# Kernel optimization log

Hardware: AMD Instinct MI355X
Metric: run time of the kernel (lower is better)

## Reference

```python
import jax, jax.numpy as jnp
import numpy as np

B, H, HKV, QLEN, KVLEN, D = 4, 32, 8, 16, 8192, 128


def setup_inputs() -> dict:
    key = jax.random.key(0)
    ks = jax.random.split(key, 7)
    query = jax.random.normal(ks[0], (B, H, QLEN, D), dtype=jnp.float32)
    # INT8 KV caches (stored as int8, dequantized in the hot path)
    key_cache = jax.random.randint(ks[1], (B, HKV, KVLEN, D), -127, 128).astype(jnp.int8)
    value_cache = jax.random.randint(ks[2], (B, HKV, KVLEN, D), -127, 128).astype(jnp.int8)
    # per-(batch, kv_head, token) quant params, broadcast over head_dim
    key_scale = jax.random.uniform(ks[3], (B, HKV, KVLEN), dtype=jnp.float32, minval=0.005, maxval=0.02)
    key_zero = jax.random.normal(ks[4], (B, HKV, KVLEN), dtype=jnp.float32)
    value_scale = jax.random.uniform(ks[5], (B, HKV, KVLEN), dtype=jnp.float32, minval=0.005, maxval=0.02)
    value_zero = jax.random.normal(ks[6], (B, HKV, KVLEN), dtype=jnp.float32)
    return {
        "query": query,
        "key_cache": key_cache,
        "value_cache": value_cache,
        "key_scale": key_scale,
        "key_zero": key_zero,
        "value_scale": value_scale,
        "value_zero": value_zero,
    }


def _dequant(x_q, scale, zero, dtype):
    # (x_q - zero) * scale, params broadcast over head_dim
    return ((x_q.astype(jnp.float32) - zero[..., None]) * scale[..., None]).astype(dtype)


def reference(query, key_cache, value_cache, key_scale, key_zero, value_scale, value_zero):
    b, h, qlen, d = query.shape
    hkv = key_cache.shape[1]
    n_rep = h // hkv  # GQA: each kv head serves n_rep query heads
    scale = jnp.asarray(d, query.dtype) ** -0.5

    k = _dequant(key_cache, key_scale, key_zero, query.dtype)   # [b, hkv, kv, d]
    v = _dequant(value_cache, value_scale, value_zero, query.dtype)

    # Grouped einsum == repeat_interleave of K/V along heads, without materializing copies
    qg = query.reshape(b, hkv, n_rep, qlen, d)
    scores = jnp.einsum('bgrqd,bgkd->bgrqk', qg, k) * scale      # [b, hkv, n_rep, q, kv]
    attn = jax.nn.softmax(scores, axis=-1)
    out = jnp.einsum('bgrqk,bgkd->bgrqd', attn, v)
    return out.reshape(b, h, qlen, d)
```

## Files before the change

kernel.cpp:

```cpp
#include <hip/hip_runtime.h>
#include <hip/hip_bf16.h>
#include <stdint.h>

#define Bc    4
#define Hc    32
#define HKVc  8
#define QLc   16
#define KVc   8192
#define Dc    128
#define NREPc 4
#define THR   8.0f

typedef _Float16 f16x8 __attribute__((ext_vector_type(8)));
typedef _Float16 f16x4 __attribute__((ext_vector_type(4)));
typedef float f32x4  __attribute__((ext_vector_type(4)));
typedef int   i32x4  __attribute__((ext_vector_type(4)));
typedef uint32_t u32x2 __attribute__((ext_vector_type(2)));

__device__ __forceinline__ uint32_t pk1152(int x0, int x1) {
  return (__builtin_amdgcn_perm((uint32_t)x1, (uint32_t)x0, 0x05040100u)
          & 0x00FF00FFu) ^ 0x64806480u;
}

#define BAR() do {                                            \
    asm volatile("s_waitcnt lgkmcnt(0)" ::: "memory");        \
    __builtin_amdgcn_sched_barrier(0);                        \
    __builtin_amdgcn_s_barrier();                             \
  } while (0)

__global__ __launch_bounds__(256) void attn_partial(
    const float* __restrict__ q, const int* __restrict__ kc,
    const int* __restrict__ vc,
    const float* __restrict__ ksc, const float* __restrict__ kzr,
    const float* __restrict__ vsc, const float* __restrict__ vzr,
    float* __restrict__ ws_acc, float* __restrict__ ws_m,
    float* __restrict__ ws_l, int nsplit)
{
  __shared__ __align__(16) unsigned short Klds[2][32][128];
  __shared__ __align__(16) unsigned short Vlds[2][128][36];
  __shared__ __align__(16) float          Sl[4][256];

  const int bid   = blockIdx.x;
  const int split = bid % nsplit;
  const int bg    = bid / nsplit;
  const int chunk = KVc / nsplit;
  const int t_begin = split * chunk;
  const int nt    = chunk >> 5;

  const int tid  = threadIdx.x;
  const int wave = tid >> 6;
  const int lane = tid & 63;
  const int l15  = lane & 15;
  const int lg   = lane >> 4;

  const int b = bg >> 3, g = bg & 7;
  const int h = (g << 2) + wave;

  f16x8 qa[4];
  float qsum = 0.f;
  const float* qrow = q + ((size_t)((b * Hc + h) * QLc + l15)) * Dc;
#pragma unroll
  for (int ks = 0; ks < 4; ++ks) {
    const f32x4* qv = (const f32x4*)(qrow + ks * 32 + (lg << 3));
    f32x4 qlo = qv[0], qhi = qv[1];
    f16x8 f;
#pragma unroll
    for (int j = 0; j < 4; ++j) {
      f[j]     = (_Float16)qlo[j];
      f[4 + j] = (_Float16)qhi[j];
      qsum += (float)f[j] + (float)f[4 + j];
    }
    qa[ks] = f;
  }
  qsum += __shfl_xor(qsum, 16);
  qsum += __shfl_xor(qsum, 32);

  const float QK_SCALE = 0.088388347648f * 1.44269504089f;

  float m = -1e30f, ell = 0.f, corr = 0.f;
  f32x4 acc[8];
#pragma unroll
  for (int dt = 0; dt < 8; ++dt) acc[dt] = (f32x4){0.f, 0.f, 0.f, 0.f};

  const int*   kb   = kc  + (size_t)bg * KVc * Dc;
  const int*   vb   = vc  + (size_t)bg * KVc * Dc;
  const float* kscb = ksc + (size_t)bg * KVc;
  const float* kzrb = kzr + (size_t)bg * KVc;
  const float* vscb = vsc + (size_t)bg * KVc;
  const float* vzrb = vzr + (size_t)bg * KVc;

  const int kt  = tid >> 3;
  const int kd  = (tid & 7) << 4;
  const int ksw = (kt & 7) << 3;
  const int tq  = tid >> 5;
  const int dq  = (tid & 31) << 2;
  const int tb  = (tq << 2) ^ ((((dq >> 4) & 3)) << 3);

  i32x4 kpA[4], vpA[4], kpB[4], vpB[4];

#define ISSUE(KP, VP, TILE) do {                                             \
    const int _t0 = t_begin + ((TILE) << 5);                                 \
    const int* _ks = kb + (size_t)(_t0 + kt) * Dc + kd;                      \
    KP[0] = ((const i32x4*)_ks)[0]; KP[1] = ((const i32x4*)_ks)[1];          \
    KP[2] = ((const i32x4*)_ks)[2]; KP[3] = ((const i32x4*)_ks)[3];          \
    VP[0] = *(const i32x4*)(vb + (size_t)(_t0 + (tq << 2) + 0) * Dc + dq);   \
    VP[1] = *(const i32x4*)(vb + (size_t)(_t0 + (tq << 2) + 1) * Dc + dq);   \
    VP[2] = *(const i32x4*)(vb + (size_t)(_t0 + (tq << 2) + 2) * Dc + dq);   \
    VP[3] = *(const i32x4*)(vb + (size_t)(_t0 + (tq << 2) + 3) * Dc + dq);   \
  } while (0)

#define WRITE(KP, VP, BUF) do {                                              \
    i32x4 _kA, _kB;                                                          \
    _kA[0]=(int)pk1152(KP[0][0],KP[0][1]); _kA[1]=(int)pk1152(KP[0][2],KP[0][3]); \
    _kA[2]=(int)pk1152(KP[1][0],KP[1][1]); _kA[3]=(int)pk1152(KP[1][2],KP[1][3]); \
    _kB[0]=(int)pk1152(KP[2][0],KP[2][1]); _kB[1]=(int)pk1152(KP[2][2],KP[2][3]); \
    _kB[2]=(int)pk1152(KP[3][0],KP[3][1]); _kB[3]=(int)pk1152(KP[3][2],KP[3][3]); \
    *(i32x4*)&Klds[BUF][kt][kd ^ ksw]       = _kA;                           \
    *(i32x4*)&Klds[BUF][kt][(kd + 8) ^ ksw] = _kB;                           \
    _Pragma("unroll")                                                        \
    for (int _j = 0; _j < 4; ++_j) {                                         \
      u32x2 _pk;                                                             \
      _pk[0] = pk1152(VP[0][_j], VP[1][_j]);                                 \
      _pk[1] = pk1152(VP[2][_j], VP[3][_j]);                                 \
      *(u32x2*)&Vlds[BUF][dq + _j][tb] = _pk;                                \
    }                                                                        \
  } while (0)

#define RESTAGE(WBASE) do {                                                  \
    const int _arr = tid >> 6;                                               \
    const int _sl  = (tid & 63) << 2;                                        \
    int _toff = _sl;                                                         \
    if (_toff > chunk - 4) _toff = chunk - 4;                                \
    const float* _sp = (_arr == 0) ? kscb : (_arr == 1) ? kzrb               \
                     : (_arr == 2) ? vscb : vzrb;                            \
    f32x4 _sv = *(const f32x4*)(_sp + (WBASE) + _toff);                      \
    if (_arr == 0) { _sv[0]*=QK_SCALE; _sv[1]*=QK_SCALE;                     \
                     _sv[2]*=QK_SCALE; _sv[3]*=QK_SCALE; }                   \
    else if (_arr == 2) { _sv[0]*=1024.f; _sv[1]*=1024.f;                    \
                          _sv[2]*=1024.f; _sv[3]*=1024.f; }                  \
    else { _sv[0]+=1152.f; _sv[1]+=1152.f; _sv[2]+=1152.f; _sv[3]+=1152.f; } \
    *(f32x4*)&Sl[_arr][_sl] = _sv;                                           \
  } while (0)

  ISSUE(kpA, vpA, 0);
  RESTAGE(t_begin);
  WRITE(kpA, vpA, 0);
  if (nt > 1) ISSUE(kpA, vpA, 1);
  if (nt > 2) ISSUE(kpB, vpB, 2);
  BAR();

  for (int it = 0; it < nt; ++it) {
    const int cur = it & 1;

    if (it && !(it & 7)) {
      RESTAGE(t_begin + ((it >> 3) << 8));
      BAR();
    }

    if (it + 1 < nt) {
      if ((it + 1) & 1) {
        WRITE(kpA, vpA, cur ^ 1);
        if (it + 3 < nt) ISSUE(kpA, vpA, it + 3);
      } else {
        WRITE(kpB, vpB, cur ^ 1);
        if (it + 3 < nt) ISSUE(kpB, vpB, it + 3);
      }
    }

    const int tw = (it & 7) << 5;
    const f32x4 ksc0 = *(const f32x4*)&Sl[0][tw + (lg << 2)];
    const f32x4 ksc1 = *(const f32x4*)&Sl[0][tw + 16 + (lg << 2)];
    const f32x4 kzr0 = *(const f32x4*)&Sl[1][tw + (lg << 2)];
    const f32x4 kzr1 = *(const f32x4*)&Sl[1][tw + 16 + (lg << 2)];
    const f32x4 vsc0 = *(const f32x4*)&Sl[2][tw + (lg << 2)];
    const f32x4 vsc1 = *(const f32x4*)&Sl[2][tw + 16 + (lg << 2)];
    const f32x4 vzr0 = *(const f32x4*)&Sl[3][tw + (lg << 2)];
    const f32x4 vzr1 = *(const f32x4*)&Sl[3][tw + 16 + (lg << 2)];

    f32x4 sA0 = (f32x4){0.f,0.f,0.f,0.f}, sA1 = (f32x4){0.f,0.f,0.f,0.f};
    f32x4 sB0 = (f32x4){0.f,0.f,0.f,0.f}, sB1 = (f32x4){0.f,0.f,0.f,0.f};
    __builtin_amdgcn_s_setprio(1);
#pragma unroll
    for (int ks = 0; ks < 2; ++ks) {
      f16x8 kfA = *(const f16x8*)
          &Klds[cur][l15][(ks * 32 + (lg << 3)) ^ ((l15 & 7) << 3)];
      sA0 = __builtin_amdgcn_mfma_f32_16x16x32_f16(kfA, qa[ks], sA0, 0, 0, 0);
      f16x8 kfB = *(const f16x8*)
          &Klds[cur][16 + l15][(ks * 32 + (lg << 3)) ^ ((l15 & 7) << 3)];
      sB0 = __builtin_amdgcn_mfma_f32_16x16x32_f16(kfB, qa[ks], sB0, 0, 0, 0);
    }
#pragma unroll
    for (int ks = 2; ks < 4; ++ks) {
      f16x8 kfA = *(const f16x8*)
          &Klds[cur][l15][(ks * 32 + (lg << 3)) ^ ((l15 & 7) << 3)];
      sA1 = __builtin_amdgcn_mfma_f32_16x16x32_f16(kfA, qa[ks], sA1, 0, 0, 0);
      f16x8 kfB = *(const f16x8*)
          &Klds[cur][16 + l15][(ks * 32 + (lg << 3)) ^ ((l15 & 7) << 3)];
      sB1 = __builtin_amdgcn_mfma_f32_16x16x32_f16(kfB, qa[ks], sB1, 0, 0, 0);
    }
    __builtin_amdgcn_s_setprio(0);
    const f32x4 scA = sA0 + sA1;
    const f32x4 scB = sB0 + sB1;

    float s0[4], s1[4];
#pragma unroll
    for (int j = 0; j < 4; ++j) {
      s0[j] = ksc0[j] * (scA[j] - kzr0[j] * qsum);
      s1[j] = ksc1[j] * (scB[j] - kzr1[j] * qsum);
    }

    float tm = fmaxf(fmaxf(fmaxf(s0[0], s0[1]), fmaxf(s0[2], s0[3])),
                     fmaxf(fmaxf(s1[0], s1[1]), fmaxf(s1[2], s1[3])));
    tm = fmaxf(tm, __shfl_xor(tm, 16));
    tm = fmaxf(tm, __shfl_xor(tm, 32));
    if (__any(tm > m + THR)) {
      float nm = fmaxf(m, tm);
      float cf = exp2f(m - nm);
      m = nm;
      ell *= cf; corr *= cf;
      float cfq[4];
#pragma unroll
      for (int j = 0; j < 4; ++j) cfq[j] = __shfl(cf, (lg << 2) + j);
#pragma unroll
      for (int dt = 0; dt < 8; ++dt)
#pragma unroll
        for (int j = 0; j < 4; ++j) acc[dt][j] *= cfq[j];
    }

    f16x8 pp;
#pragma unroll
    for (int j = 0; j < 4; ++j) {
      float pA = exp2f(s0[j] - m);
      float pB = exp2f(s1[j] - m);
      ell += pA + pB;
      _Float16 ca = (_Float16)(pA * vsc0[j]);
      _Float16 cb = (_Float16)(pB * vsc1[j]);
      corr += (float)ca * vzr0[j] + (float)cb * vzr1[j];
      pp[j]     = ca;
      pp[4 + j] = cb;
    }

    __builtin_amdgcn_s_setprio(1);
#pragma unroll
    for (int dt = 0; dt < 8; ++dt) {
      const int swz = (dt & 3) << 3;
      f16x4 vA = *(const f16x4*)&Vlds[cur][(dt << 4) + l15][(lg << 2) ^ swz];
      f16x4 vB = *(const f16x4*)&Vlds[cur][(dt << 4) + l15][(16 + (lg << 2)) ^ swz];
      f16x8 vf = __builtin_shufflevector(vA, vB, 0, 1, 2, 3, 4, 5, 6, 7);
      acc[dt] = __builtin_amdgcn_mfma_f32_16x16x32_f16(pp, vf, acc[dt], 0, 0, 0);
    }
    __builtin_amdgcn_s_setprio(0);

    if (it + 1 < nt) BAR();
  }

  ell += __shfl_xor(ell, 16);  ell += __shfl_xor(ell, 32);
  corr += __shfl_xor(corr, 16); corr += __shfl_xor(corr, 32);
  float corrq[4];
#pragma unroll
  for (int j = 0; j < 4; ++j) corrq[j] = __shfl(corr, (lg << 2) + j);

  const size_t pbase = ((size_t)bg * nsplit + split) * 64;
  const float inv1k = 0.0009765625f;
#pragma unroll
  for (int dt = 0; dt < 8; ++dt)
#pragma unroll
    for (int j = 0; j < 4; ++j) {
      int row = (wave << 4) + (lg << 2) + j;
      int d   = (dt << 4) + l15;
      ws_acc[(pbase + row) * Dc + d] = (acc[dt][j] - corrq[j]) * inv1k;
    }
  if (lg == 0) {
    ws_m[pbase + (wave << 4) + l15] = m;
    ws_l[pbase + (wave << 4) + l15] = ell;
  }
#undef ISSUE
#undef WRITE
#undef RESTAGE
}

__global__ __launch_bounds__(128) void attn_combine(
    const float* __restrict__ ws_acc, const float* __restrict__ ws_m,
    const float* __restrict__ ws_l, float* __restrict__ out, int nsplit)
{
  const int r   = blockIdx.x;
  const int bg  = r >> 6;
  const int row = r & 63;
  const int d   = threadIdx.x;

  float M = -1e30f;
#pragma unroll 4
  for (int i = 0; i < nsplit; ++i)
    M = fmaxf(M, ws_m[((size_t)bg * nsplit + i) * 64 + row]);
  float L = 0.f, o = 0.f;
#pragma unroll 4
  for (int i = 0; i < nsplit; ++i) {
    size_t pb = ((size_t)bg * nsplit + i) * 64 + row;
    float w = exp2f(ws_m[pb] - M);
    L += ws_l[pb] * w;
    o += ws_acc[pb * Dc + d] * w;
  }
  const int b = bg >> 3, g = bg & 7;
  const int rep = row >> 4, qq = row & 15;
  out[(((size_t)(b * Hc + g * NREPc + rep)) * QLc + qq) * Dc + d] = o / L;
}

extern "C" void kernel_launch(void* const* d_in, const int* in_sizes, int n_in,
                              void* d_out, int out_size, void* d_ws,
                              size_t ws_size, hipStream_t stream) {
  const float* q   = (const float*)d_in[0];
  const int*   kc  = (const int*)d_in[1];
  const int*   vc  = (const int*)d_in[2];
  const float* ksc = (const float*)d_in[3];
  const float* kzr = (const float*)d_in[4];
  const float* vsc = (const float*)d_in[5];
  const float* vzr = (const float*)d_in[6];
  float* out = (float*)d_out;

  int nsplit = 32;
  while (nsplit > 1) {
    size_t need = (size_t)32 * nsplit * 64 * (Dc + 2) * sizeof(float);
    if (need <= ws_size) break;
    nsplit >>= 1;
  }
  float* ws_acc = (float*)d_ws;
  float* ws_m   = ws_acc + (size_t)32 * nsplit * 64 * Dc;
  float* ws_l   = ws_m   + (size_t)32 * nsplit * 64;

  attn_partial<<<dim3(32 * nsplit), dim3(256), 0, stream>>>(
      q, kc, vc, ksc, kzr, vsc, vzr, ws_acc, ws_m, ws_l, nsplit);
  attn_combine<<<dim3(32 * 64), dim3(128), 0, stream>>>(
      ws_acc, ws_m, ws_l, out, nsplit);
}
```

Before: 80.88 us.

## Process 64 KV tokens per iteration using both LDS buffers as one tile

```diff
diff --git a/kernel.cpp b/kernel.cpp
--- a/kernel.cpp
+++ b/kernel.cpp
@@ -45,7 +45,7 @@
   const int bg    = bid / nsplit;
   const int chunk = KVc / nsplit;
   const int t_begin = split * chunk;
-  const int nt    = chunk >> 5;
+  const int nt2   = chunk >> 6;
 
   const int tid  = threadIdx.x;
   const int wave = tid >> 6;
@@ -143,74 +143,59 @@
   } while (0)
 
   ISSUE(kpA, vpA, 0);
+  ISSUE(kpB, vpB, 1);
   RESTAGE(t_begin);
   WRITE(kpA, vpA, 0);
-  if (nt > 1) ISSUE(kpA, vpA, 1);
-  if (nt > 2) ISSUE(kpB, vpB, 2);
+  WRITE(kpB, vpB, 1);
+  if (nt2 > 1) { ISSUE(kpA, vpA, 2); ISSUE(kpB, vpB, 3); }
   BAR();
 
-  for (int it = 0; it < nt; ++it) {
-    const int cur = it & 1;
-
-    if (it && !(it & 7)) {
-      RESTAGE(t_begin + ((it >> 3) << 8));
+  for (int st = 0; st < nt2; ++st) {
+    if (st && !(st & 3)) {
+      RESTAGE(t_begin + ((st >> 2) << 8));
       BAR();
     }
 
-    if (it + 1 < nt) {
-      if ((it + 1) & 1) {
-        WRITE(kpA, vpA, cur ^ 1);
-        if (it + 3 < nt) ISSUE(kpA, vpA, it + 3);
-      } else {
-        WRITE(kpB, vpB, cur ^ 1);
-        if (it + 3 < nt) ISSUE(kpB, vpB, it + 3);
-      }
-    }
-
-    const int tw = (it & 7) << 5;
+    const int tw = (st & 3) << 6;
     const f32x4 ksc0 = *(const f32x4*)&Sl[0][tw + (lg << 2)];
     const f32x4 ksc1 = *(const f32x4*)&Sl[0][tw + 16 + (lg << 2)];
+    const f32x4 ksc2 = *(const f32x4*)&Sl[0][tw + 32 + (lg << 2)];
+    const f32x4 ksc3 = *(const f32x4*)&Sl[0][tw + 48 + (lg << 2)];
     const f32x4 kzr0 = *(const f32x4*)&Sl[1][tw + (lg << 2)];
     const f32x4 kzr1 = *(const f32x4*)&Sl[1][tw + 16 + (lg << 2)];
-    const f32x4 vsc0 = *(const f32x4*)&Sl[2][tw + (lg << 2)];
-    const f32x4 vsc1 = *(const f32x4*)&Sl[2][tw + 16 + (lg << 2)];
-    const f32x4 vzr0 = *(const f32x4*)&Sl[3][tw + (lg << 2)];
-    const f32x4 vzr1 = *(const f32x4*)&Sl[3][tw + 16 + (lg << 2)];
-
-    f32x4 sA0 = (f32x4){0.f,0.f,0.f,0.f}, sA1 = (f32x4){0.f,0.f,0.f,0.f};
-    f32x4 sB0 = (f32x4){0.f,0.f,0.f,0.f}, sB1 = (f32x4){0.f,0.f,0.f,0.f};
+    const f32x4 kzr2 = *(const f32x4*)&Sl[1][tw + 32 + (lg << 2)];
+    const f32x4 kzr3 = *(const f32x4*)&Sl[1][tw + 48 + (lg << 2)];
+
+    f32x4 sc0 = (f32x4){0.f,0.f,0.f,0.f}, sc1 = (f32x4){0.f,0.f,0.f,0.f};
+    f32x4 sc2 = (f32x4){0.f,0.f,0.f,0.f}, sc3 = (f32x4){0.f,0.f,0.f,0.f};
     __builtin_amdgcn_s_setprio(1);
 #pragma unroll
-    for (int ks = 0; ks < 2; ++ks) {
-      f16x8 kfA = *(const f16x8*)
-          &Klds[cur][l15][(ks * 32 + (lg << 3)) ^ ((l15 & 7) << 3)];
-      sA0 = __builtin_amdgcn_mfma_f32_16x16x32_f16(kfA, qa[ks], sA0, 0, 0, 0);
-      f16x8 kfB = *(const f16x8*)
-          &Klds[cur][16 + l15][(ks * 32 + (lg << 3)) ^ ((l15 & 7) << 3)];
-      sB0 = __builtin_amdgcn_mfma_f32_16x16x32_f16(kfB, qa[ks], sB0, 0, 0, 0);
-    }
-#pragma unroll
-    for (int ks = 2; ks < 4; ++ks) {
-      f16x8 kfA = *(const f16x8*)
-          &Klds[cur][l15][(ks * 32 + (lg << 3)) ^ ((l15 & 7) << 3)];
-      sA1 = __builtin_amdgcn_mfma_f32_16x16x32_f16(kfA, qa[ks], sA1, 0, 0, 0);
-      f16x8 kfB = *(const f16x8*)
-          &Klds[cur][16 + l15][(ks * 32 + (lg << 3)) ^ ((l15 & 7) << 3)];
-      sB1 = __builtin_amdgcn_mfma_f32_16x16x32_f16(kfB, qa[ks], sB1, 0, 0, 0);
+    for (int ks = 0; ks < 4; ++ks) {
+      const int ko = (ks * 32 + (lg << 3)) ^ ((l15 & 7) << 3);
+      f16x8 kf0 = *(const f16x8*)&Klds[0][l15][ko];
+      sc0 = __builtin_amdgcn_mfma_f32_16x16x32_f16(kf0, qa[ks], sc0, 0, 0, 0);
+      f16x8 kf1 = *(const f16x8*)&Klds[0][16 + l15][ko];
+      sc1 = __builtin_amdgcn_mfma_f32_16x16x32_f16(kf1, qa[ks], sc1, 0, 0, 0);
+      f16x8 kf2 = *(const f16x8*)&Klds[1][l15][ko];
+      sc2 = __builtin_amdgcn_mfma_f32_16x16x32_f16(kf2, qa[ks], sc2, 0, 0, 0);
+      f16x8 kf3 = *(const f16x8*)&Klds[1][16 + l15][ko];
+      sc3 = __builtin_amdgcn_mfma_f32_16x16x32_f16(kf3, qa[ks], sc3, 0, 0, 0);
     }
     __builtin_amdgcn_s_setprio(0);
-    const f32x4 scA = sA0 + sA1;
-    const f32x4 scB = sB0 + sB1;
-
-    float s0[4], s1[4];
+
+    float s0[4], s1[4], s2[4], s3[4];
 #pragma unroll
     for (int j = 0; j < 4; ++j) {
-      s0[j] = ksc0[j] * (scA[j] - kzr0[j] * qsum);
-      s1[j] = ksc1[j] * (scB[j] - kzr1[j] * qsum);
+      s0[j] = ksc0[j] * (sc0[j] - kzr0[j] * qsum);
+      s1[j] = ksc1[j] * (sc1[j] - kzr1[j] * qsum);
+      s2[j] = ksc2[j] * (sc2[j] - kzr2[j] * qsum);
+      s3[j] = ksc3[j] * (sc3[j] - kzr3[j] * qsum);
     }
 
     float tm = fmaxf(fmaxf(fmaxf(s0[0], s0[1]), fmaxf(s0[2], s0[3])),
                      fmaxf(fmaxf(s1[0], s1[1]), fmaxf(s1[2], s1[3])));
+    tm = fmaxf(tm, fmaxf(fmaxf(fmaxf(s2[0], s2[1]), fmaxf(s2[2], s2[3])),
+                         fmaxf(fmaxf(s3[0], s3[1]), fmaxf(s3[2], s3[3]))));
     tm = fmaxf(tm, __shfl_xor(tm, 16));
     tm = fmaxf(tm, __shfl_xor(tm, 32));
     if (__any(tm > m + THR)) {
@@ -227,31 +212,57 @@
         for (int j = 0; j < 4; ++j) acc[dt][j] *= cfq[j];
     }
 
-    f16x8 pp;
+    const f32x4 vsc0 = *(const f32x4*)&Sl[2][tw + (lg << 2)];
+    const f32x4 vsc1 = *(const f32x4*)&Sl[2][tw + 16 + (lg << 2)];
+    const f32x4 vsc2 = *(const f32x4*)&Sl[2][tw + 32 + (lg << 2)];
+    const f32x4 vsc3 = *(const f32x4*)&Sl[2][tw + 48 + (lg << 2)];
+    const f32x4 vzr0 = *(const f32x4*)&Sl[3][tw + (lg << 2)];
+    const f32x4 vzr1 = *(const f32x4*)&Sl[3][tw + 16 + (lg << 2)];
+    const f32x4 vzr2 = *(const f32x4*)&Sl[3][tw + 32 + (lg << 2)];
+    const f32x4 vzr3 = *(const f32x4*)&Sl[3][tw + 48 + (lg << 2)];
+    f16x8 ppA, ppB;
 #pragma unroll
     for (int j = 0; j < 4; ++j) {
-      float pA = exp2f(s0[j] - m);
-      float pB = exp2f(s1[j] - m);
-      ell += pA + pB;
-      _Float16 ca = (_Float16)(pA * vsc0[j]);
-      _Float16 cb = (_Float16)(pB * vsc1[j]);
-      corr += (float)ca * vzr0[j] + (float)cb * vzr1[j];
-      pp[j]     = ca;
-      pp[4 + j] = cb;
+      float p0 = exp2f(s0[j] - m);
+      float p1 = exp2f(s1[j] - m);
+      float p2 = exp2f(s2[j] - m);
+      float p3 = exp2f(s3[j] - m);
+      ell += (p0 + p1) + (p2 + p3);
+      _Float16 c0 = (_Float16)(p0 * vsc0[j]);
+      _Float16 c1 = (_Float16)(p1 * vsc1[j]);
+      _Float16 c2 = (_Float16)(p2 * vsc2[j]);
+      _Float16 c3 = (_Float16)(p3 * vsc3[j]);
+      corr += ((float)c0 * vzr0[j] + (float)c1 * vzr1[j])
+            + ((float)c2 * vzr2[j] + (float)c3 * vzr3[j]);
+      ppA[j] = c0; ppA[4 + j] = c1;
+      ppB[j] = c2; ppB[4 + j] = c3;
     }
 
     __builtin_amdgcn_s_setprio(1);
 #pragma unroll
     for (int dt = 0; dt < 8; ++dt) {
       const int swz = (dt & 3) << 3;
-      f16x4 vA = *(const f16x4*)&Vlds[cur][(dt << 4) + l15][(lg << 2) ^ swz];
-      f16x4 vB = *(const f16x4*)&Vlds[cur][(dt << 4) + l15][(16 + (lg << 2)) ^ swz];
-      f16x8 vf = __builtin_shufflevector(vA, vB, 0, 1, 2, 3, 4, 5, 6, 7);
-      acc[dt] = __builtin_amdgcn_mfma_f32_16x16x32_f16(pp, vf, acc[dt], 0, 0, 0);
+      f16x4 vA0 = *(const f16x4*)&Vlds[0][(dt << 4) + l15][(lg << 2) ^ swz];
+      f16x4 vA1 = *(const f16x4*)&Vlds[0][(dt << 4) + l15][(16 + (lg << 2)) ^ swz];
+      f16x8 vfA = __builtin_shufflevector(vA0, vA1, 0, 1, 2, 3, 4, 5, 6, 7);
+      acc[dt] = __builtin_amdgcn_mfma_f32_16x16x32_f16(ppA, vfA, acc[dt], 0, 0, 0);
+      f16x4 vB0 = *(const f16x4*)&Vlds[1][(dt << 4) + l15][(lg << 2) ^ swz];
+      f16x4 vB1 = *(const f16x4*)&Vlds[1][(dt << 4) + l15][(16 + (lg << 2)) ^ swz];
+      f16x8 vfB = __builtin_shufflevector(vB0, vB1, 0, 1, 2, 3, 4, 5, 6, 7);
+      acc[dt] = __builtin_amdgcn_mfma_f32_16x16x32_f16(ppB, vfB, acc[dt], 0, 0, 0);
     }
     __builtin_amdgcn_s_setprio(0);
 
-    if (it + 1 < nt) BAR();
+    if (st + 1 < nt2) {
+      BAR();
+      WRITE(kpA, vpA, 0);
+      WRITE(kpB, vpB, 1);
+      if (st + 2 < nt2) {
+        ISSUE(kpA, vpA, ((st + 2) << 1));
+        ISSUE(kpB, vpB, ((st + 2) << 1) + 1);
+      }
+      BAR();
+    }
   }
 
   ell += __shfl_xor(ell, 16);  ell += __shfl_xor(ell, 32);
```

After: 92.44 us. +14.3%, slower.
